# Performance work log

Hardware: AMD Instinct MI355X
Metric: run time of the kernel (lower is better)

Reference implementation:

```python
import jax, jax.numpy as jnp
import numpy as np

EPS_SUM = 1e-5   # clamp on soft-assignment mass
EPS_NORM = 1e-12  # F.normalize eps


def setup_inputs() -> dict:
    key = jax.random.key(0)
    k1, k2, k3 = jax.random.split(key, 3)
    bs, ch, h, w = 64, 256, 56, 56
    num_parts = 3
    featmaps = jax.random.normal(k1, (bs, ch, h, w), dtype=jnp.float32)
    # kaiming-normal-like init for centers, clamped positive as in init_parameters
    part_centers = jnp.clip(
        jax.random.normal(k2, (num_parts, ch), dtype=jnp.float32) * np.sqrt(2.0 / ch),
        1e-5, None)
    part_smooth_factors = jax.random.normal(k3, (num_parts,), dtype=jnp.float32) * 0.1
    return {"featmaps": featmaps, "part_centers": part_centers,
            "part_smooth_factors": part_smooth_factors}


def reference(featmaps, part_centers, part_smooth_factors):
    bs, ch, h, w = featmaps.shape
    k = part_centers.shape[0]
    x = featmaps.reshape(bs, ch, h * w)                      # [bs, ch, n]

    # distance terms
    cx = jnp.einsum('kc,bcn->bkn', part_centers, x)          # [bs, k, n]
    x_sq = jnp.sum(x * x, axis=1, keepdims=True)             # [bs, 1, n]
    c_sq = jnp.sum(part_centers * part_centers, axis=1)      # [k]

    beta = jax.nn.sigmoid(part_smooth_factors)               # [k]
    logits = jnp.minimum(2.0 * cx - x_sq - c_sq[None, :, None], 0.0) / beta[None, :, None]
    assign = jax.nn.softmax(logits, axis=1)                  # softmax over parts, [bs, k, n]

    # weighted pooling
    qx = jnp.einsum('bkn,bcn->bkc', assign, x)               # [bs, k, ch]
    sum_ass = jnp.maximum(jnp.sum(assign, axis=2, keepdims=True), EPS_SUM)  # [bs, k, 1]
    qx_ = qx / sum_ass

    sigma = jnp.sqrt(beta / 2.0)                             # [k]
    out = (qx_ - part_centers[None]) / sigma[None, :, None]  # [bs, k, ch]
    norm = jnp.maximum(jnp.linalg.norm(out, axis=2, keepdims=True), EPS_NORM)
    outputs = (out / norm).transpose(0, 2, 1)                # [bs, ch, k]

    return outputs, assign.reshape(bs, k, h, w)
```

## Files before the change

### kernel.cpp

```cpp
#include <hip/hip_runtime.h>
#include <math.h>

#define BS   64
#define CH   256
#define NPIX 3136
#define NK   3
#define P    64
#define NT   49
#define XPAD 68

#define WS_SA 0
#define WS_QX (BS*NK)

__global__ __launch_bounds__(256)
void pgn_main(const float* __restrict__ x,
              const float* __restrict__ centers,
              const float* __restrict__ psf,
              float* __restrict__ assign_out,
              float* __restrict__ sa,
              float* __restrict__ qx)
{
    __shared__ float  x_sh[CH * XPAD];
    __shared__ float4 ctr_sh[CH];
    __shared__ float  part[4][16][16];
    __shared__ float  a_sh[NK][P];
    __shared__ float  cred[4][NK];
    __shared__ float  csq_sh[NK];

    const int tid  = threadIdx.x;
    const int b    = blockIdx.x / NT;
    const int t    = blockIdx.x % NT;
    const int n0   = t * P;
    const int pq   = tid & 15;
    const int cc   = tid >> 4;
    const int lane = tid & 63;
    const int w    = tid >> 6;

    {
        const float c0 = centers[tid], c1 = centers[CH + tid], c2 = centers[2*CH + tid];
        ctr_sh[tid] = make_float4(c0, c1, c2, 0.f);
        float s0 = c0*c0, s1 = c1*c1, s2 = c2*c2;
        #pragma unroll
        for (int m = 32; m; m >>= 1) {
            s0 += __shfl_xor(s0, m, 64);
            s1 += __shfl_xor(s1, m, 64);
            s2 += __shfl_xor(s2, m, 64);
        }
        if (lane == 0) { cred[w][0] = s0; cred[w][1] = s1; cred[w][2] = s2; }
    }
    __syncthreads();
    if (tid < NK) csq_sh[tid] = cred[0][tid] + cred[1][tid] + cred[2][tid] + cred[3][tid];

    float cxa[NK][4], xsq[4];
    #pragma unroll
    for (int j = 0; j < 4; ++j) { cxa[0][j]=0.f; cxa[1][j]=0.f; cxa[2][j]=0.f; xsq[j]=0.f; }

    const float* xb = x + (size_t)b * CH * NPIX + (n0 + 4*pq);
    #pragma unroll
    for (int i = 0; i < 16; ++i) {
        const int c = 16*i + cc;
        const float4 xv = *(const float4*)(xb + (size_t)c * NPIX);
        ((float4*)(x_sh + c * XPAD))[pq] = xv;
        const float4 cv = ctr_sh[c];
        const float xj[4] = {xv.x, xv.y, xv.z, xv.w};
        #pragma unroll
        for (int j = 0; j < 4; ++j) {
            cxa[0][j] = fmaf(cv.x, xj[j], cxa[0][j]);
            cxa[1][j] = fmaf(cv.y, xj[j], cxa[1][j]);
            cxa[2][j] = fmaf(cv.z, xj[j], cxa[2][j]);
            xsq[j]    = fmaf(xj[j], xj[j], xsq[j]);
        }
    }

    #pragma unroll
    for (int j = 0; j < 4; ++j) {
        #pragma unroll
        for (int k = 0; k < NK; ++k) {
            cxa[k][j] += __shfl_xor(cxa[k][j], 16, 64);
            cxa[k][j] += __shfl_xor(cxa[k][j], 32, 64);
        }
        xsq[j] += __shfl_xor(xsq[j], 16, 64);
        xsq[j] += __shfl_xor(xsq[j], 32, 64);
    }
    if ((tid & 48) == 0) {
        float* pp = &part[w][pq][0];
        #pragma unroll
        for (int j = 0; j < 4; ++j) {
            pp[j]      = cxa[0][j];
            pp[4 + j]  = cxa[1][j];
            pp[8 + j]  = cxa[2][j];
            pp[12 + j] = xsq[j];
        }
    }
    __syncthreads();

    if (tid < P) {
        const int p = tid, q = p >> 2, r = p & 3;
        float cx0 = 0.f, cx1 = 0.f, cx2 = 0.f, xs = 0.f;
        #pragma unroll
        for (int ww = 0; ww < 4; ++ww) {
            cx0 += part[ww][q][r];
            cx1 += part[ww][q][4 + r];
            cx2 += part[ww][q][8 + r];
            xs  += part[ww][q][12 + r];
        }
        const float rb0 = 1.f + __expf(-psf[0]);
        const float rb1 = 1.f + __expf(-psf[1]);
        const float rb2 = 1.f + __expf(-psf[2]);
        const float l0 = fminf(2.f*cx0 - xs - csq_sh[0], 0.f) * rb0;
        const float l1 = fminf(2.f*cx1 - xs - csq_sh[1], 0.f) * rb1;
        const float l2 = fminf(2.f*cx2 - xs - csq_sh[2], 0.f) * rb2;
        const float m  = fmaxf(l0, fmaxf(l1, l2));
        const float e0 = __expf(l0 - m), e1 = __expf(l1 - m), e2 = __expf(l2 - m);
        const float inv = 1.f / (e0 + e1 + e2);
        const float a0 = e0*inv, a1 = e1*inv, a2 = e2*inv;

        a_sh[0][p] = a0; a_sh[1][p] = a1; a_sh[2][p] = a2;

        float* ao = assign_out + (size_t)b * NK * NPIX + n0 + p;
        ao[0]        = a0;
        ao[NPIX]     = a1;
        ao[2*NPIX]   = a2;

        float s0 = a0, s1 = a1, s2 = a2;
        #pragma unroll
        for (int m2 = 32; m2; m2 >>= 1) {
            s0 += __shfl_xor(s0, m2, 64);
            s1 += __shfl_xor(s1, m2, 64);
            s2 += __shfl_xor(s2, m2, 64);
        }
        if (tid == 0) {
            atomicAdd(&sa[b*NK + 0], s0);
            atomicAdd(&sa[b*NK + 1], s1);
            atomicAdd(&sa[b*NK + 2], s2);
        }
    }
    __syncthreads();

    float q0 = 0.f, q1 = 0.f, q2 = 0.f;
    const float4* xr = (const float4*)(x_sh + tid * XPAD);
    const float4* A0 = (const float4*)&a_sh[0][0];
    const float4* A1 = (const float4*)&a_sh[1][0];
    const float4* A2 = (const float4*)&a_sh[2][0];
    #pragma unroll
    for (int i = 0; i < 16; ++i) {
        const float4 xv  = xr[i];
        const float4 a0v = A0[i], a1v = A1[i], a2v = A2[i];
        q0 = fmaf(a0v.x, xv.x, fmaf(a0v.y, xv.y, fmaf(a0v.z, xv.z, fmaf(a0v.w, xv.w, q0))));
        q1 = fmaf(a1v.x, xv.x, fmaf(a1v.y, xv.y, fmaf(a1v.z, xv.z, fmaf(a1v.w, xv.w, q1))));
        q2 = fmaf(a2v.x, xv.x, fmaf(a2v.y, xv.y, fmaf(a2v.z, xv.z, fmaf(a2v.w, xv.w, q2))));
    }
    float* qb = qx + (size_t)b * NK * CH + tid;
    atomicAdd(qb,        q0);
    atomicAdd(qb + CH,   q1);
    atomicAdd(qb + 2*CH, q2);
}

__global__ __launch_bounds__(256)
void pgn_final(const float* __restrict__ qx,
               const float* __restrict__ sa,
               const float* __restrict__ centers,
               const float* __restrict__ psf,
               float* __restrict__ out)
{
    const int b = blockIdx.x;
    const int c = threadIdx.x;
    const int wave = c >> 6, lane = c & 63;
    __shared__ float red[4][NK];
    __shared__ float nrm[NK];

    float v[NK], ss[NK];
    #pragma unroll
    for (int k = 0; k < NK; ++k) {
        const float beta = 1.f / (1.f + __expf(-psf[k]));
        const float sig  = sqrtf(0.5f * beta);
        const float s    = fmaxf(sa[b*NK + k], 1e-5f);
        const float q    = qx[((size_t)b*NK + k)*CH + c] / s;
        v[k]  = (q - centers[k*CH + c]) / sig;
        ss[k] = v[k] * v[k];
    }
    #pragma unroll
    for (int m = 32; m; m >>= 1) {
        ss[0] += __shfl_xor(ss[0], m, 64);
        ss[1] += __shfl_xor(ss[1], m, 64);
        ss[2] += __shfl_xor(ss[2], m, 64);
    }
    if (lane == 0) { red[wave][0] = ss[0]; red[wave][1] = ss[1]; red[wave][2] = ss[2]; }
    __syncthreads();
    if (c < NK) {
        const float tot = red[0][c] + red[1][c] + red[2][c] + red[3][c];
        nrm[c] = fmaxf(sqrtf(tot), 1e-12f);
    }
    __syncthreads();
    float* o = out + ((size_t)b*CH + c)*NK;
    #pragma unroll
    for (int k = 0; k < NK; ++k) o[k] = v[k] / nrm[k];
}

extern "C" void kernel_launch(void* const* d_in, const int* in_sizes, int n_in,
                              void* d_out, int out_size, void* d_ws, size_t ws_size,
                              hipStream_t stream)
{
    const float* feat    = (const float*)d_in[0];
    const float* centers = (const float*)d_in[1];
    const float* psf     = (const float*)d_in[2];

    float* out        = (float*)d_out;
    float* assign_out = out + (size_t)BS*CH*NK;

    float* sa = (float*)d_ws + WS_SA;
    float* qx = (float*)d_ws + WS_QX;

    hipMemsetAsync(d_ws, 0, (BS*NK + BS*NK*CH) * sizeof(float), stream);

    pgn_main<<<dim3(BS*NT), dim3(256), 0, stream>>>(
        feat, centers, psf, assign_out, sa, qx);

    pgn_final<<<dim3(BS), dim3(256), 0, stream>>>(qx, sa, centers, psf, out);
}
```

Before: 299.3 us.

## Drop shared-memory x tile; reload x from global and reduce via butterfly shuffles

The 68 KB shared-memory copy of the x tile is removed. The pooling phase now re-reads x from global memory, which should mostly hit in L2 or cache, and computes per-thread partial products. A transpose-style butterfly shuffle across the 16 pixel-groups then reduces these partial products per channel. This cuts LDS use sharply, which should raise occupancy, at the cost of a second global read of the tile and extra shuffle instructions.

Measured after the change: 308.9 us. 3.2% more time.

```diff
diff --git a/kernel.cpp b/kernel.cpp
--- a/kernel.cpp
+++ b/kernel.cpp
@@ -7,7 +7,6 @@
 #define NK   3
 #define P    64
 #define NT   49
-#define XPAD 68
 
 #define WS_SA 0
 #define WS_QX (BS*NK)
@@ -20,7 +19,6 @@
               float* __restrict__ sa,
               float* __restrict__ qx)
 {
-    __shared__ float  x_sh[CH * XPAD];
     __shared__ float4 ctr_sh[CH];
     __shared__ float  part[4][16][16];
     __shared__ float  a_sh[NK][P];
@@ -60,7 +58,6 @@
     for (int i = 0; i < 16; ++i) {
         const int c = 16*i + cc;
         const float4 xv = *(const float4*)(xb + (size_t)c * NPIX);
-        ((float4*)(x_sh + c * XPAD))[pq] = xv;
         const float4 cv = ctr_sh[c];
         const float xj[4] = {xv.x, xv.y, xv.z, xv.w};
         #pragma unroll
@@ -137,23 +134,66 @@
     }
     __syncthreads();
 
-    float q0 = 0.f, q1 = 0.f, q2 = 0.f;
-    const float4* xr = (const float4*)(x_sh + tid * XPAD);
-    const float4* A0 = (const float4*)&a_sh[0][0];
-    const float4* A1 = (const float4*)&a_sh[1][0];
-    const float4* A2 = (const float4*)&a_sh[2][0];
+    float ar[NK][4];
+    #pragma unroll
+    for (int k = 0; k < NK; ++k)
+        #pragma unroll
+        for (int j = 0; j < 4; ++j) ar[k][j] = a_sh[k][4*pq + j];
+
+    float q[16][NK];
     #pragma unroll
     for (int i = 0; i < 16; ++i) {
-        const float4 xv  = xr[i];
-        const float4 a0v = A0[i], a1v = A1[i], a2v = A2[i];
-        q0 = fmaf(a0v.x, xv.x, fmaf(a0v.y, xv.y, fmaf(a0v.z, xv.z, fmaf(a0v.w, xv.w, q0))));
-        q1 = fmaf(a1v.x, xv.x, fmaf(a1v.y, xv.y, fmaf(a1v.z, xv.z, fmaf(a1v.w, xv.w, q1))));
-        q2 = fmaf(a2v.x, xv.x, fmaf(a2v.y, xv.y, fmaf(a2v.z, xv.z, fmaf(a2v.w, xv.w, q2))));
-    }
-    float* qb = qx + (size_t)b * NK * CH + tid;
-    atomicAdd(qb,        q0);
-    atomicAdd(qb + CH,   q1);
-    atomicAdd(qb + 2*CH, q2);
+        const int c = 16*i + cc;
+        const float4 xv = *(const float4*)(xb + (size_t)c * NPIX);
+        q[i][0] = fmaf(ar[0][0], xv.x, fmaf(ar[0][1], xv.y, fmaf(ar[0][2], xv.z, ar[0][3]*xv.w)));
+        q[i][1] = fmaf(ar[1][0], xv.x, fmaf(ar[1][1], xv.y, fmaf(ar[1][2], xv.z, ar[1][3]*xv.w)));
+        q[i][2] = fmaf(ar[2][0], xv.x, fmaf(ar[2][1], xv.y, fmaf(ar[2][2], xv.z, ar[2][3]*xv.w)));
+    }
+
+    const bool b0 = (pq & 1) != 0;
+    float c1v[8][NK];
+    #pragma unroll
+    for (int u = 0; u < 8; ++u)
+        #pragma unroll
+        for (int k = 0; k < NK; ++k) {
+            const float send = b0 ? q[2*u][k]   : q[2*u+1][k];
+            const float keep = b0 ? q[2*u+1][k] : q[2*u][k];
+            c1v[u][k] = keep + __shfl_xor(send, 1, 64);
+        }
+    const bool b1 = (pq & 2) != 0;
+    float c2v[4][NK];
+    #pragma unroll
+    for (int u = 0; u < 4; ++u)
+        #pragma unroll
+        for (int k = 0; k < NK; ++k) {
+            const float send = b1 ? c1v[2*u][k]   : c1v[2*u+1][k];
+            const float keep = b1 ? c1v[2*u+1][k] : c1v[2*u][k];
+            c2v[u][k] = keep + __shfl_xor(send, 2, 64);
+        }
+    const bool b2 = (pq & 4) != 0;
+    float c3v[2][NK];
+    #pragma unroll
+    for (int u = 0; u < 2; ++u)
+        #pragma unroll
+        for (int k = 0; k < NK; ++k) {
+            const float send = b2 ? c2v[2*u][k]   : c2v[2*u+1][k];
+            const float keep = b2 ? c2v[2*u+1][k] : c2v[2*u][k];
+            c3v[u][k] = keep + __shfl_xor(send, 4, 64);
+        }
+    const bool b3 = (pq & 8) != 0;
+    float r[NK];
+    #pragma unroll
+    for (int k = 0; k < NK; ++k) {
+        const float send = b3 ? c3v[0][k] : c3v[1][k];
+        const float keep = b3 ? c3v[1][k] : c3v[0][k];
+        r[k] = keep + __shfl_xor(send, 8, 64);
+    }
+
+    const int c_out = 16*pq + cc;
+    float* qb = qx + (size_t)b * NK * CH + c_out;
+    atomicAdd(qb,        r[0]);
+    atomicAdd(qb + CH,   r[1]);
+    atomicAdd(qb + 2*CH, r[2]);
 }
 
 __global__ __launch_bounds__(256)
```

## Enlarge pixel tile to 256 and reread x from global instead of LDS

Applied to the files above, without the earlier changes.

Each block now covers 256 pixels instead of 64, so there are 13 tiles per image and about a quarter as many atomics on qx and sa. The x tile is no longer staged in shared memory. The first pass reads it with coalesced float4 loads per wave, and the weighted-pooling pass reads it again from global, relying on L2/cache hits. The assignment-mass reduction goes through shared memory, and assignment outputs use nontemporal stores. The risks are the second global read of x, a ragged last tile, and fewer blocks to fill the GPU.

After: 324.3 us. 8.4% more time.

```diff
diff --git a/kernel.cpp b/kernel.cpp
--- a/kernel.cpp
+++ b/kernel.cpp
@@ -5,12 +5,13 @@
 #define CH   256
 #define NPIX 3136
 #define NK   3
-#define P    64
-#define NT   49
-#define XPAD 68
+#define TILE 256
+#define NT   13
 
 #define WS_SA 0
 #define WS_QX (BS*NK)
+
+typedef float f32x4 __attribute__((ext_vector_type(4)));
 
 __global__ __launch_bounds__(256)
 void pgn_main(const float* __restrict__ x,
@@ -20,21 +21,20 @@
               float* __restrict__ sa,
               float* __restrict__ qx)
 {
-    __shared__ float  x_sh[CH * XPAD];
     __shared__ float4 ctr_sh[CH];
-    __shared__ float  part[4][16][16];
-    __shared__ float  a_sh[NK][P];
+    __shared__ float  part[16*4*64];
+    __shared__ float  a_sh[NK][TILE];
     __shared__ float  cred[4][NK];
     __shared__ float  csq_sh[NK];
+    __shared__ float  sred[4][NK];
 
     const int tid  = threadIdx.x;
     const int b    = blockIdx.x / NT;
     const int t    = blockIdx.x % NT;
-    const int n0   = t * P;
-    const int pq   = tid & 15;
-    const int cc   = tid >> 4;
+    const int n0   = t * TILE;
+    const int tlen = (NPIX - n0 < TILE) ? (NPIX - n0) : TILE;
+    const int w    = tid >> 6;
     const int lane = tid & 63;
-    const int w    = tid >> 6;
 
     {
         const float c0 = centers[tid], c1 = centers[CH + tid], c2 = centers[2*CH + tid];
@@ -55,72 +55,69 @@
     #pragma unroll
     for (int j = 0; j < 4; ++j) { cxa[0][j]=0.f; cxa[1][j]=0.f; cxa[2][j]=0.f; xsq[j]=0.f; }
 
-    const float* xb = x + (size_t)b * CH * NPIX + (n0 + 4*pq);
-    #pragma unroll
-    for (int i = 0; i < 16; ++i) {
-        const int c = 16*i + cc;
-        const float4 xv = *(const float4*)(xb + (size_t)c * NPIX);
-        ((float4*)(x_sh + c * XPAD))[pq] = xv;
-        const float4 cv = ctr_sh[c];
-        const float xj[4] = {xv.x, xv.y, xv.z, xv.w};
-        #pragma unroll
-        for (int j = 0; j < 4; ++j) {
-            cxa[0][j] = fmaf(cv.x, xj[j], cxa[0][j]);
-            cxa[1][j] = fmaf(cv.y, xj[j], cxa[1][j]);
-            cxa[2][j] = fmaf(cv.z, xj[j], cxa[2][j]);
-            xsq[j]    = fmaf(xj[j], xj[j], xsq[j]);
-        }
-    }
-
-    #pragma unroll
-    for (int j = 0; j < 4; ++j) {
-        #pragma unroll
-        for (int k = 0; k < NK; ++k) {
-            cxa[k][j] += __shfl_xor(cxa[k][j], 16, 64);
-            cxa[k][j] += __shfl_xor(cxa[k][j], 32, 64);
-        }
-        xsq[j] += __shfl_xor(xsq[j], 16, 64);
-        xsq[j] += __shfl_xor(xsq[j], 32, 64);
-    }
-    if ((tid & 48) == 0) {
-        float* pp = &part[w][pq][0];
-        #pragma unroll
-        for (int j = 0; j < 4; ++j) {
-            pp[j]      = cxa[0][j];
-            pp[4 + j]  = cxa[1][j];
-            pp[8 + j]  = cxa[2][j];
-            pp[12 + j] = xsq[j];
-        }
-    }
-    __syncthreads();
-
-    if (tid < P) {
+    const int c0g = w * 64;
+    const bool lv = (4*lane) < tlen;
+    const float* xrow = x + (size_t)b * CH * NPIX + n0 + (lv ? 4*lane : 0);
+
+    #pragma unroll 2
+    for (int cu = 0; cu < 64; cu += 8) {
+        f32x4 xv8[8];
+        #pragma unroll
+        for (int u = 0; u < 8; ++u)
+            xv8[u] = *(const f32x4*)(xrow + (size_t)(c0g + cu + u) * NPIX);
+        #pragma unroll
+        for (int u = 0; u < 8; ++u) {
+            const float4 cv = ctr_sh[c0g + cu + u];
+            #pragma unroll
+            for (int j = 0; j < 4; ++j) {
+                const float xj = xv8[u][j];
+                cxa[0][j] = fmaf(cv.x, xj, cxa[0][j]);
+                cxa[1][j] = fmaf(cv.y, xj, cxa[1][j]);
+                cxa[2][j] = fmaf(cv.z, xj, cxa[2][j]);
+                xsq[j]    = fmaf(xj, xj, xsq[j]);
+            }
+        }
+    }
+
+    #pragma unroll
+    for (int k = 0; k < NK; ++k)
+        #pragma unroll
+        for (int j = 0; j < 4; ++j)
+            part[(k*4 + j)*256 + w*64 + lane] = cxa[k][j];
+    #pragma unroll
+    for (int j = 0; j < 4; ++j)
+        part[(12 + j)*256 + w*64 + lane] = xsq[j];
+    __syncthreads();
+
+    float a0 = 0.f, a1 = 0.f, a2 = 0.f;
+    {
         const int p = tid, q = p >> 2, r = p & 3;
-        float cx0 = 0.f, cx1 = 0.f, cx2 = 0.f, xs = 0.f;
-        #pragma unroll
-        for (int ww = 0; ww < 4; ++ww) {
-            cx0 += part[ww][q][r];
-            cx1 += part[ww][q][4 + r];
-            cx2 += part[ww][q][8 + r];
-            xs  += part[ww][q][12 + r];
-        }
-        const float rb0 = 1.f + __expf(-psf[0]);
-        const float rb1 = 1.f + __expf(-psf[1]);
-        const float rb2 = 1.f + __expf(-psf[2]);
-        const float l0 = fminf(2.f*cx0 - xs - csq_sh[0], 0.f) * rb0;
-        const float l1 = fminf(2.f*cx1 - xs - csq_sh[1], 0.f) * rb1;
-        const float l2 = fminf(2.f*cx2 - xs - csq_sh[2], 0.f) * rb2;
-        const float m  = fmaxf(l0, fmaxf(l1, l2));
-        const float e0 = __expf(l0 - m), e1 = __expf(l1 - m), e2 = __expf(l2 - m);
-        const float inv = 1.f / (e0 + e1 + e2);
-        const float a0 = e0*inv, a1 = e1*inv, a2 = e2*inv;
-
+        if (p < tlen) {
+            float cx0 = 0.f, cx1 = 0.f, cx2 = 0.f, xs = 0.f;
+            #pragma unroll
+            for (int ww = 0; ww < 4; ++ww) {
+                cx0 += part[(0  + r)*256 + ww*64 + q];
+                cx1 += part[(4  + r)*256 + ww*64 + q];
+                cx2 += part[(8  + r)*256 + ww*64 + q];
+                xs  += part[(12 + r)*256 + ww*64 + q];
+            }
+            const float rb0 = 1.f + __expf(-psf[0]);
+            const float rb1 = 1.f + __expf(-psf[1]);
+            const float rb2 = 1.f + __expf(-psf[2]);
+            const float l0 = fminf(2.f*cx0 - xs - csq_sh[0], 0.f) * rb0;
+            const float l1 = fminf(2.f*cx1 - xs - csq_sh[1], 0.f) * rb1;
+            const float l2 = fminf(2.f*cx2 - xs - csq_sh[2], 0.f) * rb2;
+            const float m  = fmaxf(l0, fmaxf(l1, l2));
+            const float e0 = __expf(l0 - m), e1 = __expf(l1 - m), e2 = __expf(l2 - m);
+            const float inv = 1.f / (e0 + e1 + e2);
+            a0 = e0*inv; a1 = e1*inv; a2 = e2*inv;
+
+            float* ao = assign_out + (size_t)b * NK * NPIX + n0 + p;
+            __builtin_nontemporal_store(a0, ao);
+            __builtin_nontemporal_store(a1, ao + NPIX);
+            __builtin_nontemporal_store(a2, ao + 2*NPIX);
+        }
         a_sh[0][p] = a0; a_sh[1][p] = a1; a_sh[2][p] = a2;
-
-        float* ao = assign_out + (size_t)b * NK * NPIX + n0 + p;
-        ao[0]        = a0;
-        ao[NPIX]     = a1;
-        ao[2*NPIX]   = a2;
 
         float s0 = a0, s1 = a1, s2 = a2;
         #pragma unroll
@@ -129,31 +126,30 @@
             s1 += __shfl_xor(s1, m2, 64);
             s2 += __shfl_xor(s2, m2, 64);
         }
-        if (tid == 0) {
-            atomicAdd(&sa[b*NK + 0], s0);
-            atomicAdd(&sa[b*NK + 1], s1);
-            atomicAdd(&sa[b*NK + 2], s2);
-        }
-    }
-    __syncthreads();
-
-    float q0 = 0.f, q1 = 0.f, q2 = 0.f;
-    const float4* xr = (const float4*)(x_sh + tid * XPAD);
-    const float4* A0 = (const float4*)&a_sh[0][0];
-    const float4* A1 = (const float4*)&a_sh[1][0];
-    const float4* A2 = (const float4*)&a_sh[2][0];
-    #pragma unroll
-    for (int i = 0; i < 16; ++i) {
-        const float4 xv  = xr[i];
-        const float4 a0v = A0[i], a1v = A1[i], a2v = A2[i];
-        q0 = fmaf(a0v.x, xv.x, fmaf(a0v.y, xv.y, fmaf(a0v.z, xv.z, fmaf(a0v.w, xv.w, q0))));
-        q1 = fmaf(a1v.x, xv.x, fmaf(a1v.y, xv.y, fmaf(a1v.z, xv.z, fmaf(a1v.w, xv.w, q1))));
-        q2 = fmaf(a2v.x, xv.x, fmaf(a2v.y, xv.y, fmaf(a2v.z, xv.z, fmaf(a2v.w, xv.w, q2))));
-    }
-    float* qb = qx + (size_t)b * NK * CH + tid;
-    atomicAdd(qb,        q0);
-    atomicAdd(qb + CH,   q1);
-    atomicAdd(qb + 2*CH, q2);
+        if (lane == 0) { sred[w][0] = s0; sred[w][1] = s1; sred[w][2] = s2; }
+    }
+    __syncthreads();
+    if (tid < NK)
+        atomicAdd(&sa[b*NK + tid], sred[0][tid] + sred[1][tid] + sred[2][tid] + sred[3][tid]);
+
+    {
+        const float* xc = x + ((size_t)b * CH + tid) * NPIX + n0;
+        float q0 = 0.f, q1 = 0.f, q2 = 0.f;
+        #pragma unroll 4
+        for (int j = 0; j < tlen; j += 4) {
+            const f32x4  v  = *(const f32x4*)(xc + j);
+            const float4 A0 = *(const float4*)&a_sh[0][j];
+            const float4 A1 = *(const float4*)&a_sh[1][j];
+            const float4 A2 = *(const float4*)&a_sh[2][j];
+            q0 = fmaf(A0.x, v.x, fmaf(A0.y, v.y, fmaf(A0.z, v.z, fmaf(A0.w, v.w, q0))));
+            q1 = fmaf(A1.x, v.x, fmaf(A1.y, v.y, fmaf(A1.z, v.z, fmaf(A1.w, v.w, q1))));
+            q2 = fmaf(A2.x, v.x, fmaf(A2.y, v.y, fmaf(A2.z, v.z, fmaf(A2.w, v.w, q2))));
+        }
+        float* qb = qx + (size_t)b * NK * CH + tid;
+        atomicAdd(qb,        q0);
+        atomicAdd(qb + CH,   q1);
+        atomicAdd(qb + 2*CH, q2);
+    }
 }
 
 __global__ __launch_bounds__(256)
@@ -211,7 +207,7 @@
     float* sa = (float*)d_ws + WS_SA;
     float* qx = (float*)d_ws + WS_QX;
 
-    hipMemsetAsync(d_ws, 0, (BS*NK + BS*NK*CH) * sizeof(float), stream);
+    (void)hipMemsetAsync(d_ws, 0, (BS*NK + BS*NK*CH) * sizeof(float), stream);
 
     pgn_main<<<dim3(BS*NT), dim3(256), 0, stream>>>(
         feat, centers, psf, assign_out, sa, qx);
```
